# Kernel tuning notes

Hardware: AMD Instinct MI355X
Metric: run time of the kernel (lower is better)

## Reference

```python
import jax, jax.numpy as jnp
import numpy as np

BETA = 0.25
NUM_CODES = 8192
DIM_LATENT = 256
BATCH = 32768


def setup_inputs() -> dict:
    key = jax.random.key(0)
    k1, k2 = jax.random.split(key)
    z_e = jax.random.normal(k1, (BATCH, DIM_LATENT), dtype=jnp.float32)
    # nn.init.uniform_(codebook.weight, -1/num_codes, 1/num_codes)
    codebook = jax.random.uniform(
        k2, (NUM_CODES, DIM_LATENT), dtype=jnp.float32,
        minval=-1.0 / NUM_CODES, maxval=1.0 / NUM_CODES,
    )
    return {"z_e": z_e, "codebook": codebook}


def reference(z_e, codebook):
    # squared L2 distances via the ||z||^2 + ||e||^2 - 2 z.e expansion
    z2 = jnp.sum(z_e * z_e, axis=1, keepdims=True)          # [B, 1]
    e2 = jnp.sum(codebook * codebook, axis=1)[None, :]       # [1, K]
    ze = jnp.einsum('bd,kd->bk', z_e, codebook)              # [B, K]
    dist = z2 + e2 - 2.0 * ze                                # [B, K]
    indices = jnp.argmin(dist, axis=1)                       # [B]
    z_q = codebook[indices]                                  # [B, d] gather

    cb_loss = jnp.mean((z_q - jax.lax.stop_gradient(z_e)) ** 2)
    commit_loss = jnp.mean((z_e - jax.lax.stop_gradient(z_q)) ** 2)
    vq_loss = cb_loss + BETA * commit_loss

    # straight-through estimator
    z_q_st = z_e + jax.lax.stop_gradient(z_q - z_e)
    return (z_q_st, indices, vq_loss, cb_loss, commit_loss)
```

## Files before the change

### kernel.cpp

```cpp
#include <hip/hip_runtime.h>

#define BATCH   32768
#define DIM     256
#define NCODES  8192
#define BETA    0.25f
#define EPS     3e-4f
#define CAND_CAP 128

typedef unsigned short ushort_t;
typedef unsigned char  uchar_t;
typedef unsigned long long u64;
typedef __attribute__((ext_vector_type(8))) short bf16x8;
typedef __attribute__((ext_vector_type(4))) float f32x4;

#define GLOAD16(gp, lp) __builtin_amdgcn_global_load_lds( \
    (const __attribute__((address_space(1))) void*)(gp), \
    (__attribute__((address_space(3))) void*)(lp), 16, 0, 0)

#define WAITVM(N) asm volatile("s_waitcnt vmcnt(" #N ")" ::: "memory")

__device__ inline ushort_t f2bf(float f) {
    union { float f; unsigned u; } v; v.f = f;
    return (ushort_t)((v.u + 0x7FFF + ((v.u >> 16) & 1)) >> 16);
}
__device__ inline ushort_t f2bf_rd(float f) {
    union { float f; unsigned u; } v; v.f = f;
    unsigned u = v.u;
    if (f < 0.0f) u += 0xFFFFu;
    return (ushort_t)(u >> 16);
}

__global__ void vq_prep_kernel(const float* __restrict__ z,
                               const float* __restrict__ cb,
                               float* __restrict__ e2, float* __restrict__ z2,
                               ushort_t* __restrict__ eh, ushort_t* __restrict__ zh,
                               float* __restrict__ loss_acc) {
    const int lane = threadIdx.x & 63;
    const int wid  = threadIdx.x >> 6;
    const int item = blockIdx.x * 4 + wid;
    const float* src;
    ushort_t* dst;
    if (item < NCODES) { src = cb + (size_t)item * DIM;            dst = eh + (size_t)item * DIM; }
    else               { src = z  + (size_t)(item - NCODES) * DIM; dst = zh + (size_t)(item - NCODES) * DIM; }
    const float4 v = *(const float4*)(src + lane * 4);
    ushort4 b; b.x = f2bf(v.x); b.y = f2bf(v.y); b.z = f2bf(v.z); b.w = f2bf(v.w);
    *(ushort4*)(dst + lane * 4) = b;
    float s = v.x * v.x + v.y * v.y + v.z * v.z + v.w * v.w;
    #pragma unroll
    for (int off = 32; off > 0; off >>= 1) s += __shfl_down(s, off, 64);
    if (lane == 0) {
        if (item < NCODES) e2[item] = s;
        else               z2[item - NCODES] = s;
    }
    if (blockIdx.x == 0 && threadIdx.x == 0) *loss_acc = 0.0f;
}

__launch_bounds__(512, 2)
__global__ void vq_screen_kernel(const ushort_t* __restrict__ zh_g,
                                 const ushort_t* __restrict__ eh_g,
                                 const float* __restrict__ e2g,
                                 ushort_t* __restrict__ tilemin_g,
                                 uchar_t* __restrict__ mask_g) {
    __shared__ ushort_t zh_s[3][8 * 512];
    __shared__ ushort_t eh_s[3][32 * 512];
    __shared__ float    e2_s[NCODES];

    const int t    = threadIdx.x;
    const int w    = t >> 6;
    const int lane = t & 63;
    const int c    = lane & 15;
    const int q    = lane >> 4;
    const int h    = w >> 2;
    const int cq   = w & 3;
    const int row0 = blockIdx.x * 128;

    #define STAGE(n_, b_) do {                                                 \
        const int ct_ = (n_) >> 3;                                             \
        const int kc_ = ((n_) & 7) * 32;                                       \
        GLOAD16(zh_g + (size_t)(row0 + w * 16 + (lane >> 2)) * DIM + kc_ + (lane & 3) * 8, \
                &zh_s[b_][w * 512]);                                           \
        _Pragma("unroll")                                                      \
        for (int s_ = 0; s_ < 4; ++s_) {                                       \
            const int c16_ = w * 4 + s_;                                       \
            GLOAD16(eh_g + (size_t)(ct_ * 512 + c16_ * 16 + (lane >> 2)) * DIM + kc_ + (lane & 3) * 8, \
                    &eh_s[b_][c16_ * 512]);                                    \
        }                                                                      \
    } while (0)

    #pragma unroll
    for (int s_ = 0; s_ < 4; ++s_)
        GLOAD16(e2g + (w * 4 + s_) * 256 + lane * 4, &e2_s[(w * 4 + s_) * 256]);
    STAGE(0, 0);
    STAGE(1, 1);

    f32x4 acc[4][8];
    for (int n = 0; n < 128; ++n) {
        const int kc_i = n & 7;
        if (kc_i == 0) {
            #pragma unroll
            for (int i = 0; i < 4; ++i)
                #pragma unroll
                for (int j = 0; j < 8; ++j) acc[i][j] = (f32x4)0.0f;
        }

        if (n < 127) { WAITVM(5); } else { WAITVM(0); }
        __builtin_amdgcn_s_barrier();
        asm volatile("" ::: "memory");

        if (n < 126) STAGE(n + 2, (n + 2) % 3);
        const int b = n % 3;

        bf16x8 a[4], bfr[8];
        #pragma unroll
        for (int i = 0; i < 4; ++i)
            a[i] = *(const bf16x8*)&zh_s[b][(h * 4 + i) * 512 + c * 32 + q * 8];
        #pragma unroll
        for (int j = 0; j < 8; ++j)
            bfr[j] = *(const bf16x8*)&eh_s[b][(cq * 8 + j) * 512 + c * 32 + q * 8];

        __builtin_amdgcn_s_setprio(1);
        #pragma unroll
        for (int i = 0; i < 4; ++i)
            #pragma unroll
            for (int j = 0; j < 8; ++j)
                acc[i][j] = __builtin_amdgcn_mfma_f32_16x16x32_bf16(a[i], bfr[j], acc[i][j], 0, 0, 0);
        __builtin_amdgcn_s_setprio(0);

        if (kc_i == 7) {
            const int ct = n >> 3;
            float e2v[8];
            #pragma unroll
            for (int j = 0; j < 8; ++j) e2v[j] = e2_s[ct * 512 + cq * 128 + j * 16 + c];

            float tm[4][4];
            #pragma unroll
            for (int i = 0; i < 4; ++i)
                #pragma unroll
                for (int reg = 0; reg < 4; ++reg) tm[i][reg] = 3.4e38f;
            #pragma unroll
            for (int i = 0; i < 4; ++i)
                #pragma unroll
                for (int j = 0; j < 8; ++j)
                    #pragma unroll
                    for (int reg = 0; reg < 4; ++reg) {
                        const float s = fmaf(-2.0f, acc[i][j][reg], e2v[j]);
                        acc[i][j][reg] = s;
                        tm[i][reg] = fminf(tm[i][reg], s);
                    }
            #pragma unroll
            for (int st = 1; st < 16; st <<= 1)
                #pragma unroll
                for (int i = 0; i < 4; ++i)
                    #pragma unroll
                    for (int reg = 0; reg < 4; ++reg)
                        tm[i][reg] = fminf(tm[i][reg], __shfl_xor(tm[i][reg], st, 64));

            const int tile = ct * 4 + cq;
            #pragma unroll
            for (int i = 0; i < 4; ++i)
                #pragma unroll
                for (int reg = 0; reg < 4; ++reg) {
                    const int row = row0 + h * 64 + i * 16 + q * 4 + reg;
                    const float thr = tm[i][reg] + EPS;
                    unsigned m8 = 0;
                    #pragma unroll
                    for (int j = 0; j < 8; ++j)
                        m8 |= (unsigned)(acc[i][j][reg] <= thr) << j;
                    mask_g[(size_t)row * 1024 + tile * 16 + c] = (uchar_t)m8;
                    if (c == 0) tilemin_g[(size_t)row * 64 + tile] = f2bf_rd(tm[i][reg]);
                }
        }
    }
    #undef STAGE
}

__device__ inline u64 vq_eval(const float* zrow, const float* __restrict__ cb,
                              const float* __restrict__ e2g, float z2v, int code) {
    const float4* z4 = (const float4*)zrow;
    const float4* e4 = (const float4*)(cb + (size_t)code * DIM);
    float acc = 0.0f;
    #pragma unroll 8
    for (int k4 = 0; k4 < DIM / 4; ++k4) {
        const float4 a = z4[k4];
        const float4 b = e4[k4];
        acc = fmaf(a.x, b.x, acc);
        acc = fmaf(a.y, b.y, acc);
        acc = fmaf(a.z, b.z, acc);
        acc = fmaf(a.w, b.w, acc);
    }
    const float S  = z2v + e2g[code];
    const float sc = fmaf(-2.0f, acc, S);
    union { float f; unsigned u; } sb; sb.f = sc;
    return ((u64)sb.u << 32) | (unsigned)code;
}

__global__ void vq_select_kernel(const float* __restrict__ z,
                                 const float* __restrict__ cb,
                                 const float* __restrict__ e2g,
                                 const float* __restrict__ z2g,
                                 const ushort_t* __restrict__ tilemin_g,
                                 const uchar_t* __restrict__ mask_g,
                                 float* __restrict__ idx_f,
                                 int* __restrict__ idx_i) {
    __shared__ float    zrow_s[4][DIM];
    __shared__ ushort_t cand_s[4][CAND_CAP];

    const int lane = threadIdx.x & 63;
    const int w    = threadIdx.x >> 6;
    const int row  = blockIdx.x * 4 + w;

    *(float4*)&zrow_s[w][lane * 4] = *(const float4*)(z + (size_t)row * DIM + lane * 4);

    union { unsigned u; float f; } tv;
    tv.u = ((unsigned)tilemin_g[(size_t)row * 64 + lane]) << 16;
    const float tm = tv.f;
    float gmin = tm;
    #pragma unroll
    for (int d = 32; d > 0; d >>= 1) gmin = fminf(gmin, __shfl_xor(gmin, d, 64));
    const float thr = gmin + EPS;

    u64 m0 = 0, m1 = 0;
    if (tm <= thr) {
        const uchar_t* mb = mask_g + (size_t)row * 1024 + lane * 16;
        m0 = *(const u64*)(mb);
        m1 = *(const u64*)(mb + 8);
    }
    const unsigned cnt = __popcll(m0) + __popcll(m1);
    unsigned inc = cnt;
    #pragma unroll
    for (int d = 1; d < 64; d <<= 1) {
        const unsigned o = __shfl_up(inc, d, 64);
        if (lane >= d) inc += o;
    }
    const unsigned excl  = inc - cnt;
    const unsigned total = __shfl(inc, 63, 64);
    const float z2v = z2g[row];
    u64 best = ~0ull;

    __syncthreads();

    unsigned slot = excl;
    while (m0) {
        const int p = __builtin_ctzll(m0); m0 &= m0 - 1;
        const unsigned code = lane * 128 + (p & 7) * 16 + (p >> 3);
        if (slot < CAND_CAP) cand_s[w][slot] = (ushort_t)code;
        else best = min(best, vq_eval(zrow_s[w], cb, e2g, z2v, (int)code));
        ++slot;
    }
    while (m1) {
        const int p = __builtin_ctzll(m1); m1 &= m1 - 1;
        const unsigned code = lane * 128 + (p & 7) * 16 + 8 + (p >> 3);
        if (slot < CAND_CAP) cand_s[w][slot] = (ushort_t)code;
        else best = min(best, vq_eval(zrow_s[w], cb, e2g, z2v, (int)code));
        ++slot;
    }

    __syncthreads();

    const int n = (int)(total < CAND_CAP ? total : CAND_CAP);
    for (int s = lane; s < n; s += 64)
        best = min(best, vq_eval(zrow_s[w], cb, e2g, z2v, (int)cand_s[w][s]));

    #pragma unroll
    for (int d = 32; d > 0; d >>= 1) {
        const u64 o = (u64)__shfl_xor((unsigned long long)best, d, 64);
        best = min(best, o);
    }
    if (lane == 0) {
        const int k = (int)(best & (u64)(NCODES - 1));
        idx_f[row] = (float)k;
        idx_i[row] = k;
    }
}

__global__ void vq_gather_loss_kernel(const float* __restrict__ z,
                                      const float* __restrict__ cb,
                                      const int* __restrict__ idx_i,
                                      float* __restrict__ zq_out,
                                      float* __restrict__ loss_acc) {
    const int lane = threadIdx.x & 63;
    const int wid  = threadIdx.x >> 6;
    const int row  = blockIdx.x * 4 + wid;
    const int k = idx_i[row];
    const float4 e  = *(const float4*)(cb + (size_t)k * DIM + lane * 4);
    const float4 zv = *(const float4*)(z + (size_t)row * DIM + lane * 4);
    const float dx = e.x - zv.x, dy = e.y - zv.y, dz = e.z - zv.z, dw = e.w - zv.w;
    float4 o;
    o.x = zv.x + dx; o.y = zv.y + dy; o.z = zv.z + dz; o.w = zv.w + dw;
    *(float4*)(zq_out + (size_t)row * DIM + lane * 4) = o;
    float s = dx * dx + dy * dy + dz * dz + dw * dw;
    #pragma unroll
    for (int off = 32; off > 0; off >>= 1) s += __shfl_down(s, off, 64);
    __shared__ float wsum[4];
    if (lane == 0) wsum[wid] = s;
    __syncthreads();
    if (threadIdx.x == 0)
        atomicAdd(loss_acc, wsum[0] + wsum[1] + wsum[2] + wsum[3]);
}

__global__ void vq_finalize_kernel(const float* __restrict__ loss_acc,
                                   float* __restrict__ out_losses) {
    const float mean = *loss_acc * (1.0f / (float)(BATCH * DIM));
    out_losses[0] = mean + BETA * mean;
    out_losses[1] = mean;
    out_losses[2] = mean;
}

extern "C" void kernel_launch(void* const* d_in, const int* in_sizes, int n_in,
                              void* d_out, int out_size, void* d_ws, size_t ws_size,
                              hipStream_t stream) {
    const float* z  = (const float*)d_in[0];
    const float* cb = (const float*)d_in[1];

    float* out    = (float*)d_out;
    float* zq     = out;
    float* idx_f  = out + (size_t)BATCH * DIM;
    float* losses = out + (size_t)BATCH * DIM + BATCH;
    uchar_t* mask = (uchar_t*)d_out;

    float*    ws        = (float*)d_ws;
    float*    loss_acc  = ws;
    float*    e2        = ws + 256;
    float*    z2        = e2 + NCODES;
    ushort_t* tilemin   = (ushort_t*)(z2 + BATCH);
    int*      idxi      = (int*)(tilemin + (size_t)BATCH * 64);
    ushort_t* zh        = (ushort_t*)(idxi + BATCH);
    ushort_t* eh        = zh + (size_t)BATCH * DIM;

    vq_prep_kernel<<<(NCODES + BATCH) / 4, 256, 0, stream>>>(z, cb, e2, z2, eh, zh, loss_acc);
    vq_screen_kernel<<<BATCH / 128, 512, 0, stream>>>(zh, eh, e2, tilemin, mask);
    vq_select_kernel<<<BATCH / 4, 256, 0, stream>>>(z, cb, e2, z2, tilemin, mask, idx_f, idxi);
    vq_gather_loss_kernel<<<BATCH / 4, 256, 0, stream>>>(z, cb, idxi, zq, loss_acc);
    vq_finalize_kernel<<<1, 1, 0, stream>>>(loss_acc, losses);
}
```

Baseline: 516.6 us.

## Split MFMA phase in halves interleaved with staged loads; linearize LDS tile layout

The screen kernel's main loop is reorganised. Each k-step now runs two half-batches of MFMAs. The global-to-LDS loads for step n+2 are split between the two halves, with barriers around each phase, so load issue overlaps compute. The staging lane mapping changes so each lane's fragment sits at lane*8 in LDS, giving contiguous, conflict-free fragment reads, and the buffer index uses a rotating counter instead of modulo. The extra barriers per iteration add synchronisation cost that could cancel out the overlap gains.

```diff
diff --git a/kernel.cpp b/kernel.cpp
--- a/kernel.cpp
+++ b/kernel.cpp
@@ -18,6 +18,7 @@
     (__attribute__((address_space(3))) void*)(lp), 16, 0, 0)
 
 #define WAITVM(N) asm volatile("s_waitcnt vmcnt(" #N ")" ::: "memory")
+#define BARRIER() do { __builtin_amdgcn_s_barrier(); asm volatile("" ::: "memory"); } while (0)
 
 __device__ inline ushort_t f2bf(float f) {
     union { float f; unsigned u; } v; v.f = f;
@@ -73,60 +74,74 @@
     const int h    = w >> 2;
     const int cq   = w & 3;
     const int row0 = blockIdx.x * 128;
-
-    #define STAGE(n_, b_) do {                                                 \
-        const int ct_ = (n_) >> 3;                                             \
-        const int kc_ = ((n_) & 7) * 32;                                       \
-        GLOAD16(zh_g + (size_t)(row0 + w * 16 + (lane >> 2)) * DIM + kc_ + (lane & 3) * 8, \
-                &zh_s[b_][w * 512]);                                           \
-        _Pragma("unroll")                                                      \
-        for (int s_ = 0; s_ < 4; ++s_) {                                       \
-            const int c16_ = w * 4 + s_;                                       \
-            GLOAD16(eh_g + (size_t)(ct_ * 512 + c16_ * 16 + (lane >> 2)) * DIM + kc_ + (lane & 3) * 8, \
-                    &eh_s[b_][c16_ * 512]);                                    \
-        }                                                                      \
-    } while (0)
+    const int srow = lane & 15;
+    const int skc  = (lane >> 4) * 8;
+
+    #define STAGE_Z(n_, b_) \
+        GLOAD16(zh_g + (size_t)(row0 + w * 16 + srow) * DIM + ((n_) & 7) * 32 + skc, \
+                &zh_s[b_][w * 512])
+    #define STAGE_E(n_, b_, s_) \
+        GLOAD16(eh_g + (size_t)((((n_) >> 3) * 512 + (w * 4 + (s_)) * 16 + srow)) * DIM + ((n_) & 7) * 32 + skc, \
+                &eh_s[b_][(w * 4 + (s_)) * 512])
 
     #pragma unroll
     for (int s_ = 0; s_ < 4; ++s_)
         GLOAD16(e2g + (w * 4 + s_) * 256 + lane * 4, &e2_s[(w * 4 + s_) * 256]);
-    STAGE(0, 0);
-    STAGE(1, 1);
+    STAGE_Z(0, 0);
+    #pragma unroll
+    for (int s_ = 0; s_ < 4; ++s_) STAGE_E(0, 0, s_);
+    STAGE_Z(1, 1);
+    #pragma unroll
+    for (int s_ = 0; s_ < 4; ++s_) STAGE_E(1, 1, s_);
+
+    WAITVM(5);
+    BARRIER();
 
     f32x4 acc[4][8];
+    int b = 0;
     for (int n = 0; n < 128; ++n) {
-        const int kc_i = n & 7;
-        if (kc_i == 0) {
+        const int bs = (b >= 1) ? (b - 1) : 2;
+        if ((n & 7) == 0) {
             #pragma unroll
             for (int i = 0; i < 4; ++i)
                 #pragma unroll
                 for (int j = 0; j < 8; ++j) acc[i][j] = (f32x4)0.0f;
         }
 
-        if (n < 127) { WAITVM(5); } else { WAITVM(0); }
-        __builtin_amdgcn_s_barrier();
-        asm volatile("" ::: "memory");
-
-        if (n < 126) STAGE(n + 2, (n + 2) % 3);
-        const int b = n % 3;
-
-        bf16x8 a[4], bfr[8];
+        bf16x8 a[4], f[4];
         #pragma unroll
         for (int i = 0; i < 4; ++i)
-            a[i] = *(const bf16x8*)&zh_s[b][(h * 4 + i) * 512 + c * 32 + q * 8];
-        #pragma unroll
-        for (int j = 0; j < 8; ++j)
-            bfr[j] = *(const bf16x8*)&eh_s[b][(cq * 8 + j) * 512 + c * 32 + q * 8];
-
+            a[i] = *(const bf16x8*)&zh_s[b][(h * 4 + i) * 512 + lane * 8];
+        #pragma unroll
+        for (int j = 0; j < 4; ++j)
+            f[j] = *(const bf16x8*)&eh_s[b][(cq * 8 + j) * 512 + lane * 8];
+        if (n < 126) { STAGE_Z(n + 2, bs); STAGE_E(n + 2, bs, 0); STAGE_E(n + 2, bs, 1); }
+        BARRIER();
         __builtin_amdgcn_s_setprio(1);
         #pragma unroll
         for (int i = 0; i < 4; ++i)
             #pragma unroll
-            for (int j = 0; j < 8; ++j)
-                acc[i][j] = __builtin_amdgcn_mfma_f32_16x16x32_bf16(a[i], bfr[j], acc[i][j], 0, 0, 0);
+            for (int j = 0; j < 4; ++j)
+                acc[i][j] = __builtin_amdgcn_mfma_f32_16x16x32_bf16(a[i], f[j], acc[i][j], 0, 0, 0);
         __builtin_amdgcn_s_setprio(0);
-
-        if (kc_i == 7) {
+        BARRIER();
+
+        bf16x8 g[4];
+        #pragma unroll
+        for (int j = 0; j < 4; ++j)
+            g[j] = *(const bf16x8*)&eh_s[b][(cq * 8 + 4 + j) * 512 + lane * 8];
+        if (n < 126) { STAGE_E(n + 2, bs, 2); STAGE_E(n + 2, bs, 3); }
+        if (n < 126) { WAITVM(5); } else if (n == 126) { WAITVM(0); }
+        BARRIER();
+        __builtin_amdgcn_s_setprio(1);
+        #pragma unroll
+        for (int i = 0; i < 4; ++i)
+            #pragma unroll
+            for (int j = 0; j < 4; ++j)
+                acc[i][j + 4] = __builtin_amdgcn_mfma_f32_16x16x32_bf16(a[i], g[j], acc[i][j + 4], 0, 0, 0);
+        __builtin_amdgcn_s_setprio(0);
+
+        if ((n & 7) == 7) {
             const int ct = n >> 3;
             float e2v[8];
             #pragma unroll
@@ -170,8 +185,11 @@
                     if (c == 0) tilemin_g[(size_t)row * 64 + tile] = f2bf_rd(tm[i][reg]);
                 }
         }
-    }
-    #undef STAGE
+        BARRIER();
+        b = (b < 2) ? (b + 1) : 0;
+    }
+    #undef STAGE_Z
+    #undef STAGE_E
 }
 
 __device__ inline u64 vq_eval(const float* zrow, const float* __restrict__ cb,
```

Measured after the change: 498.1 us. 1.04x faster.
